# Optimization experiments

Hardware: AMD Instinct MI355X
Metric: run time of the kernel (lower is better)

## Reference

```python
import jax, jax.numpy as jnp
import numpy as np

EPS = 1e-6

def elu1(x):
    return jax.nn.elu(x) + 1.0

def causal_linear_attention(q, k, v, chunk=128):
    # q,k,v: [b,h,s,d]; standard (elu+1) linear attention with causal cumulative
    # normalization, computed chunk-wise with a lax.scan carrying the kv state.
    b, h, s, d = q.shape
    sq, sk = elu1(q), elu1(k)
    nc = s // chunk
    rs = lambda x: x.reshape(b, h, nc, chunk, d).transpose(2, 0, 1, 3, 4)  # [nc,b,h,L,d]
    sqc, skc, vc = rs(sq), rs(sk), rs(v)
    mask = jnp.tril(jnp.ones((chunk, chunk), dtype=q.dtype))

    def step(carry, xs):
        S, z = carry  # S: [b,h,d,d] running sum of k^T v; z: [b,h,d] running sum of k
        qc, kc, vcc = xs
        scores = jnp.einsum('bhid,bhjd->bhij', qc, kc) * mask
        num = jnp.einsum('bhij,bhje->bhie', scores, vcc) + jnp.einsum('bhid,bhde->bhie', qc, S)
        den = scores.sum(-1) + jnp.einsum('bhid,bhd->bhi', qc, z)
        out = num / jnp.clip(den, EPS)[..., None]
        S = S + jnp.einsum('bhjd,bhje->bhde', kc, vcc)
        z = z + kc.sum(2)
        return (S, z), out

    S0 = jnp.zeros((b, h, d, d), q.dtype)
    z0 = jnp.zeros((b, h, d), q.dtype)
    _, outs = jax.lax.scan(step, (S0, z0), (sqc, skc, vc))
    return outs.transpose(1, 2, 0, 3, 4).reshape(b, h, s, d)

def setup_inputs() -> dict:
    B, S, H, NH, NM = 2, 4096, 2048, 16, 4
    HD = H // NH
    key = jax.random.key(0)
    ks = jax.random.split(key, 12)
    p = lambda k, shp: (jax.random.normal(k, shp, dtype=jnp.float32) * 0.02)
    return {
        'hidden_states': jax.random.normal(ks[0], (B, S, H), dtype=jnp.float32),
        'w_q': p(ks[1], (H, H)),
        'w_k': p(ks[2], (H, H)),
        'w_v': p(ks[3], (H, H)),
        'w_o': p(ks[4], (H, H)),
        'eg_w1': p(ks[5], (H // 4, H)),
        'eg_b1': jnp.zeros((H // 4,), jnp.float32),
        'eg_w2': p(ks[6], (1, H // 4)),
        'eg_b2': jnp.zeros((1,), jnp.float32),
        'memory_gate': jnp.zeros((NH,), jnp.float32),
        'fine_memories': jax.random.uniform(ks[7], (NM, NH, HD, HD), dtype=jnp.float32) * 0.1,
        'fine_memory_norms': jax.random.uniform(ks[8], (NM, NH, HD), dtype=jnp.float32) + 0.1,
    }

def reference(hidden_states, w_q, w_k, w_v, w_o, eg_w1, eg_b1, eg_w2, eg_b2,
              memory_gate, fine_memories, fine_memory_norms):
    B, S, H = hidden_states.shape
    NH = memory_gate.shape[0]
    HD = H // NH
    split = lambda x: x.reshape(B, S, NH, HD).transpose(0, 2, 1, 3)  # [b,h,s,d]
    q = split(hidden_states @ w_q.T)
    k = split(hidden_states @ w_k.T)
    v = split(hidden_states @ w_v.T)
    sq = elu1(q)

    # coarse memory = sum of fine banks
    M = fine_memories.sum(0)            # [h,d,d]
    z = fine_memory_norms.sum(0)        # [h,d]
    a_c = jnp.einsum('bhsd,hde->bhse', sq, M)
    n_c = jnp.clip(jnp.einsum('bhsd,hd->bhs', sq, z), EPS)[..., None]
    out_coarse = jnp.where(z.sum() < EPS, 0.0, a_c / n_c)

    # fine-grained retrieval over banks, softmax-weighted by relevance
    a_f = jnp.einsum('bhsd,mhde->mbhse', sq, fine_memories)
    n_f = jnp.einsum('bhsd,mhd->mbhs', sq, fine_memory_norms)
    bank_dead = (fine_memory_norms.sum((1, 2)) < EPS)[:, None, None, None, None]
    outs = jnp.where(bank_dead, 0.0, a_f / jnp.clip(n_f, EPS)[..., None])
    rel = n_f.mean(-1)  # [m,b,h]
    w = jax.nn.softmax(rel, axis=0)[..., None, None]  # [m,b,h,1,1]
    out_fine = (outs * w).sum(0)

    # learned expansion gate from coarse representation
    coarse_repr = out_coarse.transpose(0, 2, 1, 3).reshape(B, S, H)
    gprob = jax.nn.sigmoid(jax.nn.relu(coarse_repr @ eg_w1.T + eg_b1) @ eg_w2.T + eg_b2)  # [b,s,1]
    exp_prob = gprob.transpose(0, 2, 1)[..., None]  # [b,1,s,1]

    memory_output = exp_prob * out_fine + (1.0 - exp_prob) * out_coarse
    local_output = causal_linear_attention(q, k, v)
    gate = jax.nn.sigmoid(memory_gate).reshape(1, NH, 1, 1)
    output = gate * memory_output + (1.0 - gate) * local_output
    output = output.transpose(0, 2, 1, 3).reshape(B, S, H)
    return output @ w_o.T
```

## Files before the change

### kernel.cpp

```cpp
#include <hip/hip_runtime.h>

typedef unsigned short ush;
typedef short s16x8 __attribute__((ext_vector_type(8)));
typedef float f32x4 __attribute__((ext_vector_type(4)));

#define Bv 2
#define Sv 4096
#define Hv 2048
#define NHv 16
#define HDv 128
#define NMv 4
#define Tv (Bv*Sv)
#define CHv 128
#define NCv (Sv/CHv)
#define EPSf 1e-6f
#define NTHc ((size_t)Tv*Hv)

__device__ __forceinline__ float b2f(ush u){ return __uint_as_float(((unsigned)u)<<16); }
__device__ __forceinline__ ush f2b(float f){
  unsigned x = __float_as_uint(f);
  return (ush)((x + 0x7fffu + ((x>>16)&1u)) >> 16);
}
__device__ __forceinline__ float lo16(unsigned u){ return b2f((ush)(u & 0xffffu)); }
__device__ __forceinline__ float hi16(unsigned u){ return b2f((ush)(u >> 16)); }
__device__ __forceinline__ unsigned pack2(float a, float b){ return (unsigned)f2b(a) | ((unsigned)f2b(b) << 16); }
__device__ __forceinline__ float elu1f(float x){ return x > 0.f ? x + 1.f : __expf(x); }
__device__ __forceinline__ float sigm(float x){ return 1.f/(1.f + __expf(-x)); }

__device__ __forceinline__ void gload_lds16(const ush* g, ush* l) {
  __builtin_amdgcn_global_load_lds((const __attribute__((address_space(1))) unsigned int*)g,
                                   (__attribute__((address_space(3))) unsigned int*)l, 16, 0, 0);
}

__global__ void probe_kernel(float* out, float val){ out[0] = val; }

__global__ __launch_bounds__(256)
void cvt_kernel(const float* __restrict__ in, ush* __restrict__ out, int n8)
{
  int i = blockIdx.x * 256 + threadIdx.x;
  if (i >= n8) return;
  const float4* p = (const float4*)in + (size_t)i*2;
  float4 x = p[0], y = p[1];
  ushort4 a; a.x=f2b(x.x); a.y=f2b(x.y); a.z=f2b(x.z); a.w=f2b(x.w);
  ushort4 b; b.x=f2b(y.x); b.y=f2b(y.y); b.z=f2b(y.z); b.w=f2b(y.w);
  *(ushort4*)(out + (size_t)i*8)     = a;
  *(ushort4*)(out + (size_t)i*8 + 4) = b;
}

__global__ __launch_bounds__(256)
void fmt_kernel(const float* __restrict__ fm, ush* __restrict__ fmt)
{
  int mh = blockIdx.x;
  const float* src = fm + (size_t)mh*HDv*HDv;
  ush* dst = fmt + (size_t)mh*HDv*HDv;
  __shared__ ush T[HDv][HDv+4];
  #pragma unroll 4
  for (int l = 0; l < 64; ++l) {
    int idx = threadIdx.x + l*256;
    int d = idx >> 7, e = idx & 127;
    T[d][e] = f2b(src[idx]);
  }
  __syncthreads();
  #pragma unroll 4
  for (int l = 0; l < 64; ++l) {
    int idx = threadIdx.x + l*256;
    int e = idx >> 7, d = idx & 127;
    dst[idx] = T[d][e];
  }
}

__global__ __launch_bounds__(256)
void tp_kernel(const ush* __restrict__ src, ush* __restrict__ dst)
{
  int blk = blockIdx.x;
  int st = blk & 31, bh = blk >> 5;
  int h = bh & 15, b = bh >> 4;
  size_t t0 = (size_t)b*Sv + st*128;
  int hcol = h*HDv;
  __shared__ __align__(16) ush T[128*128];
  int tid = threadIdx.x;
  #pragma unroll
  for (int l = 0; l < 8; ++l) {
    int idx = tid + l*256;
    int row = idx >> 4, c8 = (idx & 15) << 3;
    *(uint4*)(T + row*128 + c8) = *(const uint4*)(src + (t0 + row)*Hv + hcol + c8);
  }
  __syncthreads();
  #pragma unroll
  for (int l = 0; l < 8; ++l) {
    int idx = tid + l*256;
    int d = idx & 127, t8 = (idx >> 7) << 3;
    ush tmp[8];
    #pragma unroll
    for (int q = 0; q < 8; ++q) tmp[q] = T[(t8 + q)*128 + d];
    *(uint4*)(dst + ((size_t)bh*HDv + d)*Sv + st*128 + t8) = *(uint4*)tmp;
  }
}

template<int OBF, int EPQ>
__global__ __launch_bounds__(512)
void gemm9(const ush* __restrict__ A, const ush* __restrict__ B,
           ush* __restrict__ C0, ush* __restrict__ C1, ush* __restrict__ C2,
           float* __restrict__ Cf, int N, int K)
{
  __shared__ __align__(16) ush LDSm[65536];
  const int tid = threadIdx.x, lane = tid & 63, w = tid >> 6;
  const int wr = w >> 2, wn = w & 3;
  const int la = lane & 15, lk = lane >> 4;

  int bid = blockIdx.x;
  int NBX = N >> 8;
  int by, bx;
  if ((NBX & 7) == 0) {
    int bpx = NBX >> 3;
    int xcd = bid & 7;
    int idx = bid >> 3;
    bx = xcd*bpx + idx % bpx;
    by = idx / bpx;
  } else {
    bx = bid % NBX;
    by = bid / NBX;
  }
  int bm = by << 8, bn = bx << 8;

  auto stageA = [&](int t, int c){
    ush* Ad = LDSm + (t & 1)*32768 + c*8192;
    int kt = t << 6;
    #pragma unroll
    for (int l = 0; l < 2; ++l) {
      int u = tid + l*512;
      int row = u >> 3, sl = u & 7;
      gload_lds16(A + (size_t)(bm + c*128 + row)*K + kt + ((sl ^ (row & 7))*8),
                  Ad + (l*512 + w*64)*8);
    }
  };
  auto stageB = [&](int t, int c){
    ush* Bd = LDSm + (t & 1)*32768 + 16384 + c*8192;
    int kt = t << 6;
    #pragma unroll
    for (int l = 0; l < 2; ++l) {
      int u = tid + l*512;
      int row = u >> 3, sl = u & 7;
      gload_lds16(B + (size_t)(bn + c*128 + row)*K + kt + ((sl ^ (row & 7))*8),
                  Bd + (l*512 + w*64)*8);
    }
  };

  f32x4 acc[8][4];
  #pragma unroll
  for (int i = 0; i < 8; ++i)
    #pragma unroll
    for (int j = 0; j < 4; ++j) acc[i][j] = (f32x4){0.f,0.f,0.f,0.f};

  stageA(0,0); stageA(0,1); stageB(0,0); stageB(0,1);
  asm volatile("s_waitcnt vmcnt(0)" ::: "memory");
  __builtin_amdgcn_s_barrier();
  __builtin_amdgcn_sched_barrier(0);

  const int nt = K >> 6;
  for (int t = 0; t < nt; ++t) {
    const ush* Ab = LDSm + (t & 1)*32768;
    const ush* Bb = Ab + 16384;
    if (t + 1 < nt) { stageA(t+1, 0); stageA(t+1, 1); }
    s16x8 b0[4], a0[4];
    __builtin_amdgcn_s_setprio(1);
    #pragma unroll
    for (int g = 0; g < 4; ++g) {
      int br = wn*64 + g*16 + la;
      b0[g] = *(const s16x8*)(Bb + br*64 + ((lk ^ (br & 7))*8));
    }
    #pragma unroll
    for (int f = 0; f < 4; ++f) {
      int ar = wr*128 + f*16 + la;
      a0[f] = *(const s16x8*)(Ab + ar*64 + ((lk ^ (ar & 7))*8));
    }
    #pragma unroll
    for (int f = 0; f < 4; ++f)
      #pragma unroll
      for (int g = 0; g < 4; ++g)
        acc[f][g] = __builtin_amdgcn_mfma_f32_16x16x32_bf16(a0[f], b0[g], acc[f][g], 0, 0, 0);
    __builtin_amdgcn_s_setprio(0);
    if (t + 1 < nt) { stageB(t+1, 0); stageB(t+1, 1); }
    __builtin_amdgcn_s_setprio(1);
    #pragma unroll
    for (int f = 0; f < 4; ++f) {
      int ar = wr*128 + (f+4)*16 + la;
      a0[f] = *(const s16x8*)(Ab + ar*64 + ((lk ^ (ar & 7))*8));
    }
    #pragma unroll
    for (int f = 0; f < 4; ++f)
      #pragma unroll
      for (int g = 0; g < 4; ++g)
        acc[f+4][g] = __builtin_amdgcn_mfma_f32_16x16x32_bf16(a0[f], b0[g], acc[f+4][g], 0, 0, 0);
    int ks1 = 4 + lk;
    #pragma unroll
    for (int g = 0; g < 4; ++g) {
      int br = wn*64 + g*16 + la;
      b0[g] = *(const s16x8*)(Bb + br*64 + ((ks1 ^ (br & 7))*8));
    }
    #pragma unroll
    for (int f = 0; f < 4; ++f) {
      int ar = wr*128 + f*16 + la;
      a0[f] = *(const s16x8*)(Ab + ar*64 + ((ks1 ^ (ar & 7))*8));
    }
    #pragma unroll
    for (int f = 0; f < 4; ++f)
      #pragma unroll
      for (int g = 0; g < 4; ++g)
        acc[f][g] = __builtin_amdgcn_mfma_f32_16x16x32_bf16(a0[f], b0[g], acc[f][g], 0, 0, 0);
    #pragma unroll
    for (int f = 0; f < 4; ++f) {
      int ar = wr*128 + (f+4)*16 + la;
      a0[f] = *(const s16x8*)(Ab + ar*64 + ((ks1 ^ (ar & 7))*8));
    }
    #pragma unroll
    for (int f = 0; f < 4; ++f)
      #pragma unroll
      for (int g = 0; g < 4; ++g)
        acc[f+4][g] = __builtin_amdgcn_mfma_f32_16x16x32_bf16(a0[f], b0[g], acc[f+4][g], 0, 0, 0);
    __builtin_amdgcn_s_setprio(0);
    __builtin_amdgcn_sched_barrier(0);
    asm volatile("s_waitcnt vmcnt(0)" ::: "memory");
    __builtin_amdgcn_s_barrier();
    __builtin_amdgcn_sched_barrier(0);
  }

  int seg = bn >> 11;
  if (OBF) {
    ush* Cb = LDSm;
    ush* outp = (seg == 0) ? C0 : (seg == 1) ? C1 : C2;
    int col0 = bn & 2047;
    #pragma unroll
    for (int h = 0; h < 2; ++h) {
      if (h) __syncthreads();
      if (wr == h) {
        #pragma unroll
        for (int f = 0; f < 8; ++f)
          #pragma unroll
          for (int g = 0; g < 4; ++g)
            #pragma unroll
            for (int r = 0; r < 4; ++r) {
              int row = f*16 + lk*4 + r;
              int col = wn*64 + g*16 + la;
              float v = acc[f][g][r];
              if (EPQ == 1 && seg < 2) v = elu1f(v);
              Cb[row*264 + col] = f2b(v);
            }
      }
      __syncthreads();
      #pragma unroll
      for (int l = 0; l < 8; ++l) {
        int chunk = tid + l*512;
        int row = chunk >> 5, cc = chunk & 31;
        *(uint4*)(outp + (size_t)(bm + h*128 + row)*2048 + col0 + cc*8) = *(const uint4*)(Cb + row*264 + cc*8);
      }
    }
  } else {
    float* Cb = (float*)LDSm;
    #pragma unroll
    for (int h2 = 0; h2 < 4; ++h2) {
      if (h2) __syncthreads();
      if (wr == (h2 >> 1)) {
        #pragma unroll
        for (int f = 0; f < 4; ++f) {
          int fa = (h2 & 1)*4 + f;
          #pragma unroll
          for (int g = 0; g < 4; ++g)
            #pragma unroll
            for (int r = 0; r < 4; ++r) {
              int row = f*16 + lk*4 + r;
              int col = wn*64 + g*16 + la;
              Cb[row*260 + col] = acc[fa][g][r];
            }
        }
      }
      __syncthreads();
      #pragma unroll
      for (int l = 0; l < 8; ++l) {
        int chunk = tid + l*512;
        int row = chunk >> 6, cc = chunk & 63;
        *(float4*)(Cf + (size_t)(bm + h2*64 + row)*N + bn + cc*4) = *(const float4*)(Cb + row*260 + cc*4);
      }
    }
  }
}

template<int OBF, int EPQ>
__global__ __launch_bounds__(512)
void gemm8(const ush* __restrict__ A, const ush* __restrict__ B,
           const float* __restrict__ bias,
           ush* __restrict__ C0, ush* __restrict__ C1, ush* __restrict__ C2,
           float* __restrict__ Cf, int N, int K)
{
  __shared__ __align__(16) ush LDS[3*16384 + 3*8192];
  ush* Atb = LDS;
  ush* Btb = LDS + 3*16384;
  const int tid = threadIdx.x, lane = tid & 63, w = tid >> 6;
  const int wr = w >> 1, wn = w & 1;
  const int la = lane & 15, lk = lane >> 4;

  int bid = blockIdx.x;
  int NBX = N >> 7;
  int by, bx;
  if ((NBX & 7) == 0) {
    int bpx = NBX >> 3;
    int xcd = bid & 7;
    int idx = bid >> 3;
    bx = xcd*bpx + idx % bpx;
    by = idx / bpx;
  } else {
    bx = bid % NBX;
    by = bid / NBX;
  }
  int bm = by << 8, bn = bx << 7;

  auto stage = [&](int t){
    int kt = t << 6;
    ush* Ad = Atb + (t % 3) * 16384;
    ush* Bd = Btb + (t % 3) * 8192;
    #pragma unroll
    for (int c = 0; c < 4; ++c) {
      int idx = tid + c*512;
      int row = idx >> 3, sl = idx & 7;
      gload_lds16(A + (size_t)(bm + row)*K + kt + ((sl ^ (row & 7))*8),
                  Ad + (w*64 + c*512)*8);
    }
    #pragma unroll
    for (int c = 0; c < 2; ++c) {
      int idx = tid + c*512;
      int row = idx >> 3, sl = idx & 7;
      gload_lds16(B + (size_t)(bn + row)*K + kt + ((sl ^ (row & 7))*8),
                  Bd + (w*64 + c*512)*8);
    }
  };

  f32x4 acc[4][4];
  #pragma unroll
  for (int i = 0; i < 4; ++i)
    #pragma unroll
    for (int j = 0; j < 4; ++j) acc[i][j] = (f32x4){0.f,0.f,0.f,0.f};

  stage(0);
  stage(1);
  const int nt = 32;
  for (int t = 0; t < nt; ++t) {
    if (t < nt-2) {
      stage(t + 2);
      asm volatile("s_waitcnt vmcnt(12)" ::: "memory");
    } else if (t == nt-2) {
      asm volatile("s_waitcnt vmcnt(6)" ::: "memory");
    } else {
      asm volatile("s_waitcnt vmcnt(0)" ::: "memory");
    }
    __builtin_amdgcn_s_barrier();
    __builtin_amdgcn_sched_barrier(0);

    const ush* Ab = Atb + (t % 3) * 16384;
    const ush* Bb = Btb + (t % 3) * 8192;
    __builtin_amdgcn_s_setprio(1);
    #pragma unroll
    for (int kk = 0; kk < 2; ++kk) {
      s16x8 a[4], b[4];
      int ks = kk*4 + lk;
      #pragma unroll
      for (int f = 0; f < 4; ++f) {
        int ar = wr*64 + f*16 + la;
        a[f] = *(const s16x8*)(Ab + ar*64 + ((ks ^ (ar & 7))*8));
        int br = wn*64 + f*16 + la;
        b[f] = *(const s16x8*)(Bb + br*64 + ((ks ^ (br & 7))*8));
      }
      #pragma unroll
      for (int i = 0; i < 4; ++i)
        #pragma unroll
        for (int j = 0; j < 4; ++j)
          acc[i][j] = __builtin_amdgcn_mfma_f32_16x16x32_bf16(a[i], b[j], acc[i][j], 0, 0, 0);
    }
    __builtin_amdgcn_s_setprio(0);
    __builtin_amdgcn_sched_barrier(0);
    __builtin_amdgcn_s_barrier();
  }

  int seg = bn >> 11;
  if (OBF) {
    ush* Cb = LDS;
    #pragma unroll
    for (int i = 0; i < 4; ++i)
      #pragma unroll
      for (int j = 0; j < 4; ++j)
        #pragma unroll
        for (int r = 0; r < 4; ++r) {
          int row = wr*64 + i*16 + lk*4 + r;
          int col = wn*64 + j*16 + la;
          float v = acc[i][j][r];
          if (EPQ == 1 && seg < 2) v = elu1f(v);
          Cb[row*136 + col] = f2b(v);
        }
    __syncthreads();
    ush* outp = (seg == 0) ? C0 : (seg == 1) ? C1 : C2;
    int col0 = bn & 2047;
    #pragma unroll
    for (int l = 0; l < 8; ++l) {
      int chunk = tid + l*512;
      int row = chunk >> 4, cc = chunk & 15;
      *(uint4*)(outp + (size_t)(bm + row)*2048 + col0 + cc*8) = *(const uint4*)(Cb + row*136 + cc*8);
    }
  } else {
    float* Cb = (float*)LDS;
    #pragma unroll
    for (int i = 0; i < 4; ++i)
      #pragma unroll
      for (int j = 0; j < 4; ++j)
        #pragma unroll
        for (int r = 0; r < 4; ++r) {
          int row = wr*64 + i*16 + lk*4 + r;
          int col = wn*64 + j*16 + la;
          float v = acc[i][j][r];
          if (EPQ == 2) v = fmaxf(v + bias[bn + col], 0.f);
          Cb[row*132 + col] = v;
        }
    __syncthreads();
    #pragma unroll
    for (int l = 0; l < 16; ++l) {
      int chunk = tid + l*512;
      int row = chunk >> 5, cc = chunk & 31;
      *(float4*)(Cf + (size_t)(bm + row)*N + bn + cc*4) = *(const float4*)(Cb + row*132 + cc*4);
    }
  }
}

__global__ void prep_kernel(const float* __restrict__ norms, const float* __restrict__ mg,
                            float* __restrict__ zsum, float* __restrict__ gate)
{
  int idx = blockIdx.x * 256 + threadIdx.x;
  if (idx < NHv*HDv) {
    float s = 0.f;
    #pragma unroll
    for (int m = 0; m < NMv; ++m) s += norms[m*NHv*HDv + idx];
    zsum[idx] = s;
  }
  if (idx < NHv) gate[idx] = sigm(mg[idx]);
}

__global__ void prep2_kernel(const float* __restrict__ norms, float* __restrict__ bdead,
                             float* __restrict__ ztot, float* __restrict__ rel)
{
  int tid = threadIdx.x;
  float pm[NMv] = {0.f,0.f,0.f,0.f};
  for (int i = tid; i < NHv*HDv; i += 256)
    #pragma unroll
    for (int m = 0; m < NMv; ++m) pm[m] += norms[m*NHv*HDv + i];
  __shared__ float red[4][NMv];
  #pragma unroll
  for (int m = 0; m < NMv; ++m) {
    float v = pm[m];
    for (int off = 32; off; off >>= 1) v += __shfl_down(v, off, 64);
    if ((tid & 63) == 0) red[tid >> 6][m] = v;
  }
  __syncthreads();
  if (tid == 0) {
    float tot = 0.f;
    #pragma unroll
    for (int m = 0; m < NMv; ++m) {
      float s = red[0][m] + red[1][m] + red[2][m] + red[3][m];
      bdead[m] = (s < EPSf) ? 1.f : 0.f;
      tot += s;
    }
    ztot[0] = tot;
  }
  if (tid < NMv*Bv*NHv) rel[tid] = 0.f;
}

__global__ __launch_bounds__(256)
void nf_kernel(const ush* __restrict__ sq, const float* __restrict__ norms,
               const float* __restrict__ zsum, float* __restrict__ nf5,
               float* __restrict__ rel)
{
  int blk = blockIdx.x;
  int st = blk % (Sv/256);
  int bh = blk / (Sv/256);
  int h = bh & 15, b = bh >> 4;
  int tid = threadIdx.x;
  __shared__ float nrm[5][HDv];
  for (int i = tid; i < 5*HDv; i += 256) {
    int m = i / HDv, d = i % HDv;
    nrm[m][d] = (m < NMv) ? norms[(m*NHv + h)*HDv + d] : zsum[h*HDv + d];
  }
  __syncthreads();
  int s = st*256 + tid;
  size_t t = (size_t)b*Sv + s;
  const ush* qp = sq + t*Hv + h*HDv;
  float acc[5] = {0.f,0.f,0.f,0.f,0.f};
  #pragma unroll 4
  for (int d0 = 0; d0 < HDv; d0 += 8) {
    uint4 u = *(const uint4*)(qp + d0);
    float q[8];
    q[0]=lo16(u.x); q[1]=hi16(u.x); q[2]=lo16(u.y); q[3]=hi16(u.y);
    q[4]=lo16(u.z); q[5]=hi16(u.z); q[6]=lo16(u.w); q[7]=hi16(u.w);
    #pragma unroll
    for (int e = 0; e < 8; ++e)
      #pragma unroll
      for (int m = 0; m < 5; ++m) acc[m] = fmaf(q[e], nrm[m][d0+e], acc[m]);
  }
  #pragma unroll
  for (int m = 0; m < 5; ++m) nf5[((size_t)m*Bv*NHv + bh)*Sv + s] = acc[m];
  __shared__ float redl[4][NMv];
  #pragma unroll
  for (int m = 0; m < NMv; ++m) {
    float v = acc[m];
    for (int off = 32; off; off >>= 1) v += __shfl_down(v, off, 64);
    if ((tid & 63) == 0) redl[tid >> 6][m] = v;
  }
  __syncthreads();
  if (tid < NMv) {
    float sm = redl[0][tid] + redl[1][tid] + redl[2][tid] + redl[3][tid];
    atomicAdd(&rel[tid*Bv*NHv + bh], sm);
  }
}

__global__ void softmax_rel(const float* __restrict__ rel, float* __restrict__ wsm)
{
  int i = threadIdx.x;
  if (i >= Bv*NHv) return;
  float r[NMv], mx = -1e30f;
  #pragma unroll
  for (int m = 0; m < NMv; ++m) { r[m] = rel[m*Bv*NHv + i] / (float)Sv; mx = fmaxf(mx, r[m]); }
  float se = 0.f;
  #pragma unroll
  for (int m = 0; m < NMv; ++m) { r[m] = __expf(r[m] - mx); se += r[m]; }
  #pragma unroll
  for (int m = 0; m < NMv; ++m) wsm[m*Bv*NHv + i] = r[m] / se;
}

__global__ __launch_bounds__(512)
void finecoarse_mfma(const ush* __restrict__ sq, const ush* __restrict__ fmt,
                     const float* __restrict__ nf5, const float* __restrict__ wsm,
                     const float* __restrict__ bdead, const float* __restrict__ ztot,
                     ush* __restrict__ fineO, ush* __restrict__ coarseO)
{
  __shared__ __align__(16) ush Qs[2*128*64];
  __shared__ __align__(16) ush Fs[2*128*64];
  __shared__ float scl[NMv][128];
  __shared__ float csc[128];

  int blk = blockIdx.x;
  int tt = blk & 31; int bh = blk >> 5;
  int h = bh & 15, b = bh >> 4;
  size_t t0 = (size_t)b*Sv + tt*128;
  int hcol = h*HDv;
  int tid = threadIdx.x;
  int lane = tid & 63, w = tid >> 6;
  int wr = w >> 2, wc = w & 3;
  int srow = lane >> 3, sslot = lane & 7;
  int la = lane & 15, lk = lane >> 4;

  #pragma unroll
  for (int kh = 0; kh < 2; ++kh)
    #pragma unroll
    for (int r = 0; r < 2; ++r) {
      int row = r*64 + w*8 + srow;
      int kg = sslot ^ (row & 7);
      gload_lds16(sq + (t0 + row)*Hv + hcol + kh*64 + kg*8,
                  Qs + kh*8192 + (r*64 + w*8)*64);
    }
  if (tid < 128) {
    int s = tt*128 + tid;
    float nc = nf5[((size_t)4*Bv*NHv + bh)*Sv + s];
    csc[tid] = (ztot[0] >= EPSf) ? 1.f/fmaxf(nc, EPSf) : 0.f;
    #pragma unroll
    for (int m = 0; m < NMv; ++m) {
      float nfm = nf5[((size_t)m*Bv*NHv + bh)*Sv + s];
      scl[m][tid] = (bdead[m] > 0.5f) ? 0.f : wsm[m*Bv*NHv + bh]/fmaxf(nfm, EPSf);
    }
  }

  f32x4 accF[4][2], accC[4][2];
  #pragma unroll
  for (int i = 0; i < 4; ++i)
    #pragma unroll
    for (int j = 0; j < 2; ++j) { accF[i][j] = (f32x4){0,0,0,0}; accC[i][j] = (f32x4){0,0,0,0}; }

  for (int m = 0; m < NMv; ++m) {
    const ush* F = fmt + (size_t)(m*NHv + h)*HDv*HDv;
    #pragma unroll
    for (int kh = 0; kh < 2; ++kh)
      #pragma unroll
      for (int r = 0; r < 2; ++r) {
        int row = r*64 + w*8 + srow;
        int kg = sslot ^ (row & 7);
        gload_lds16(F + (size_t)row*HDv + kh*64 + kg*8,
                    Fs + kh*8192 + (r*64 + w*8)*64);
      }
    __syncthreads();
    f32x4 P[4][2];
    #pragma unroll
    for (int i = 0; i < 4; ++i)
      #pragma unroll
      for (int j = 0; j < 2; ++j) P[i][j] = (f32x4){0,0,0,0};
    #pragma unroll
    for (int kh = 0; kh < 2; ++kh)
      #pragma unroll
      for (int ks = 0; ks < 2; ++ks) {
        s16x8 a[4], bq[2];
        int kslot = ks*4 + lk;
        #pragma unroll
        for (int f = 0; f < 4; ++f) {
          int arow = wr*64 + f*16 + la;
          a[f] = *(const s16x8*)(Qs + kh*8192 + arow*64 + ((kslot ^ (arow & 7))*8));
        }
        #pragma unroll
        for (int f = 0; f < 2; ++f) {
          int brow = wc*32 + f*16 + la;
          bq[f] = *(const s16x8*)(Fs + kh*8192 + brow*64 + ((kslot ^ (brow & 7))*8));
        }
        #pragma unroll
        for (int i = 0; i < 4; ++i)
          #pragma unroll
          for (int j = 0; j < 2; ++j)
            P[i][j] = __builtin_amdgcn_mfma_f32_16x16x32_bf16(a[i], bq[j], P[i][j], 0, 0, 0);
      }
    #pragma unroll
    for (int i = 0; i < 4; ++i) {
      float sm[4];
      #pragma unroll
      for (int r = 0; r < 4; ++r) sm[r] = scl[m][wr*64 + i*16 + lk*4 + r];
      #pragma unroll
      for (int j = 0; j < 2; ++j)
        #pragma unroll
        for (int r = 0; r < 4; ++r) {
          accF[i][j][r] = fmaf(sm[r], P[i][j][r], accF[i][j][r]);
          accC[i][j][r] += P[i][j][r];
        }
    }
    __syncthreads();
  }
  #pragma unroll
  for (int i = 0; i < 4; ++i)
    #pragma unroll
    for (int r = 0; r < 4; ++r) {
      int row = wr*64 + i*16 + lk*4 + r;
      float cs = csc[row];
      size_t gro = (t0 + row)*Hv + hcol;
      #pragma unroll
      for (int j = 0; j < 2; ++j) {
        int col = wc*32 + j*16 + la;
        fineO[gro + col]   = f2b(accF[i][j][r]);
        coarseO[gro + col] = f2b(accC[i][j][r]*cs);
      }
    }
}

__global__ __launch_bounds__(64)
void gprob_kernel(const float* __restrict__ g1, const float* __restrict__ w2,
                  const float* __restrict__ b2, float* __restrict__ gprob)
{
  int t = blockIdx.x, l = threadIdx.x;
  float s = 0.f;
  #pragma unroll
  for (int i = l; i < Hv/4; i += 64) s = fmaf(g1[(size_t)t*(Hv/4) + i], w2[i], s);
  for (int off = 32; off; off >>= 1) s += __shfl_down(s, off, 64);
  if (l == 0) gprob[t] = sigm(s + b2[0]);
}

__global__ __launch_bounds__(512)
void kv_chunk_mfma(const ush* __restrict__ kT, const ush* __restrict__ vT,
                   float* __restrict__ KVc, float* __restrict__ zc)
{
  __shared__ __align__(16) ush Vt[128*128];
  __shared__ __align__(16) ush Kt[128*128];
  int blk = blockIdx.x;
  int c = blk & 31, bh = blk >> 5;
  const ush* kg = kT + (size_t)bh*HDv*Sv + c*CHv;
  const ush* vg = vT + (size_t)bh*HDv*Sv + c*CHv;
  int tid = threadIdx.x, lane = tid & 63, w = tid >> 6;
  int wr = w >> 2, wc = w & 3;
  int la = lane & 15, lk = lane >> 4;
  int srow4 = lane >> 4, sslot = lane & 15;

  #pragma unroll
  for (int r = 0; r < 4; ++r) {
    int row = r*32 + w*4 + srow4;
    int slot = sslot ^ (row & 7);
    gload_lds16(vg + (size_t)row*Sv + slot*8, Vt + (r*32 + w*4)*128);
    gload_lds16(kg + (size_t)row*Sv + slot*8, Kt + (r*32 + w*4)*128);
  }
  __syncthreads();

  if (tid < 128) {
    float zacc = 0.f;
    int rx = tid & 7;
    #pragma unroll
    for (int s = 0; s < 16; ++s) {
      const ush* p = Kt + tid*128 + ((s ^ rx)*8);
      #pragma unroll
      for (int q = 0; q < 8; ++q) zacc += b2f(p[q]);
    }
    zc[(size_t)blk*HDv + tid] = zacc;
  }

  f32x4 acc[4][2];
  #pragma unroll
  for (int i = 0; i < 4; ++i)
    #pragma unroll
    for (int j = 0; j < 2; ++j) acc[i][j] = (f32x4){0,0,0,0};
  #pragma unroll
  for (int kw = 0; kw < 4; ++kw) {
    s16x8 a[4], b[2];
    int slot = kw*4 + lk;
    #pragma unroll
    for (int f = 0; f < 4; ++f) {
      int ar = wr*64 + f*16 + la;
      a[f] = *(const s16x8*)(Vt + ar*128 + ((slot ^ (ar & 7))*8));
    }
    #pragma unroll
    for (int f = 0; f < 2; ++f) {
      int br = wc*32 + f*16 + la;
      b[f] = *(const s16x8*)(Kt + br*128 + ((slot ^ (br & 7))*8));
    }
    #pragma unroll
    for (int i = 0; i < 4; ++i)
      #pragma unroll
      for (int j = 0; j < 2; ++j)
        acc[i][j] = __builtin_amdgcn_mfma_f32_16x16x32_bf16(a[i], b[j], acc[i][j], 0, 0, 0);
  }
  size_t obase = (size_t)blk*(HDv*HDv);
  #pragma unroll
  for (int i = 0; i < 4; ++i)
    #pragma unroll
    for (int j = 0; j < 2; ++j)
      #pragma unroll
      for (int r = 0; r < 4; ++r) {
        int e = wr*64 + i*16 + lk*4 + r;
        int d = wc*32 + j*16 + la;
        KVc[obase + e*HDv + d] = acc[i][j][r];
      }
}

__global__ __launch_bounds__(256)
void scan_kernel(const float* __restrict__ KVc, ush* __restrict__ kvt, float* __restrict__ zc)
{
  int blk = blockIdx.x;
  int dg = blk & 7; int bh = blk >> 3;
  int tid = threadIdx.x;
  float Sreg[8];
  #pragma unroll
  for (int k = 0; k < 8; ++k) Sreg[k] = 0.f;
  float zreg = 0.f;
  for (int c = 0; c < NCv; ++c) {
    size_t base = ((size_t)bh*NCv + c)*(HDv*HDv) + dg*2048;
    #pragma unroll
    for (int k = 0; k < 8; ++k) {
      size_t idx = base + tid + k*256;
      float tmp = KVc[idx];
      kvt[idx] = f2b(Sreg[k]);
      Sreg[k] += tmp;
    }
    if (dg == 0 && tid < HDv) {
      size_t zb = ((size_t)bh*NCv + c)*HDv + tid;
      float tmp = zc[zb];
      zc[zb] = zreg;
      zreg += tmp;
    }
  }
}

__global__ __launch_bounds__(512)
void attn_chunk_mfma(const ush* __restrict__ sq, const ush* __restrict__ sk,
                     const ush* __restrict__ vT, const ush* __restrict__ kvt,
                     const float* __restrict__ zc, ush* __restrict__ outl)
{
  __shared__ __align__(16) ush Qs[128*128];
  __shared__ __align__(16) ush Ks[128*128];
  __shared__ __align__(16) ush Vs[128*128];
  __shared__ __align__(16) ush Ss[128*128];
  __shared__ float densP[4][128];
  __shared__ float dens[128];

  int blk = blockIdx.x;
  int c = blk & 31, bh = blk >> 5;
  int h = bh & 15, b = bh >> 4;
  size_t t0 = (size_t)b*Sv + c*CHv;
  int hcol = h*HDv;
  int tid = threadIdx.x, lane = tid & 63, w = tid >> 6;
  int wr = w >> 2, wc = w & 3;
  int la = lane & 15, lk = lane >> 4;
  int srow4 = lane >> 4, sslot = lane & 15;
  const float* zcg = zc + (size_t)blk*HDv;

  const ush* qg = sq + t0*Hv + hcol;
  const ush* kg = sk + t0*Hv + hcol;
  const ush* vg = vT + (size_t)bh*HDv*Sv + c*CHv;
  const ush* sg = kvt + (size_t)blk*(HDv*HDv);
  #pragma unroll
  for (int r = 0; r < 4; ++r) {
    int row = r*32 + w*4 + srow4;
    int slot = sslot ^ (row & 7);
    int lb = (r*32 + w*4)*128;
    gload_lds16(qg + (size_t)row*Hv + slot*8, Qs + lb);
    gload_lds16(kg + (size_t)row*Hv + slot*8, Ks + lb);
    gload_lds16(vg + (size_t)row*Sv + slot*8, Vs + lb);
    gload_lds16(sg + row*HDv + slot*8, Ss + lb);
  }
  __syncthreads();

  f32x4 sc[4][2];
  #pragma unroll
  for (int i = 0; i < 4; ++i)
    #pragma unroll
    for (int j = 0; j < 2; ++j) sc[i][j] = (f32x4){0,0,0,0};
  #pragma unroll
  for (int kw = 0; kw < 4; ++kw) {
    s16x8 a[4], b[2];
    int slot = kw*4 + lk;
    #pragma unroll
    for (int f = 0; f < 4; ++f) {
      int ar = wr*64 + f*16 + la;
      a[f] = *(const s16x8*)(Qs + ar*128 + ((slot ^ (ar & 7))*8));
    }
    #pragma unroll
    for (int f = 0; f < 2; ++f) {
      int br = wc*32 + f*16 + la;
      b[f] = *(const s16x8*)(Ks + br*128 + ((slot ^ (br & 7))*8));
    }
    #pragma unroll
    for (int i = 0; i < 4; ++i)
      #pragma unroll
      for (int j = 0; j < 2; ++j)
        sc[i][j] = __builtin_amdgcn_mfma_f32_16x16x32_bf16(a[i], b[j], sc[i][j], 0, 0, 0);
  }
  __syncthreads();
  #pragma unroll
  for (int i = 0; i < 4; ++i)
    #pragma unroll
    for (int j = 0; j < 2; ++j)
      #pragma unroll
      for (int r = 0; r < 4; ++r) {
        int ii = wr*64 + i*16 + lk*4 + r;
        int jj = wc*32 + j*16 + la;
        float v = (jj <= ii) ? sc[i][j][r] : 0.f;
        Ks[ii*128 + (((jj >> 3) ^ (ii & 7))*8) + (jj & 7)] = f2b(v);
      }
  __syncthreads();

  {
    int row = tid & 127, qt = tid >> 7;
    int rx = row & 7;
    float s = 0.f;
    #pragma unroll
    for (int s8 = 0; s8 < 4; ++s8) {
      int slot = qt*4 + s8;
      const ush* p  = Ks + row*128 + ((slot ^ rx)*8);
      const ush* pq = Qs + row*128 + ((slot ^ rx)*8);
      #pragma unroll
      for (int q = 0; q < 8; ++q) s += b2f(p[q]);
      #pragma unroll
      for (int q = 0; q < 8; ++q) s = fmaf(b2f(pq[q]), zcg[slot*8 + q], s);
    }
    densP[qt][row] = s;
  }
  __syncthreads();
  if (tid < 128)
    dens[tid] = fmaxf(densP[0][tid] + densP[1][tid] + densP[2][tid] + densP[3][tid], EPSf);
  __syncthreads();

  f32x4 acc[4][2];
  #pragma unroll
  for (int i = 0; i < 4; ++i)
    #pragma unroll
    for (int j = 0; j < 2; ++j) acc[i][j] = (f32x4){0,0,0,0};
  #pragma unroll
  for (int kw = 0; kw < 4; ++kw) {
    s16x8 a[4], b[2];
    int slot = kw*4 + lk;
    #pragma unroll
    for (int f = 0; f < 4; ++f) {
      int ar = wr*64 + f*16 + la;
      a[f] = *(const s16x8*)(Ks + ar*128 + ((slot ^ (ar & 7))*8));
    }
    #pragma unroll
    for (int f = 0; f < 2; ++f) {
      int br = wc*32 + f*16 + la;
      b[f] = *(const s16x8*)(Vs + br*128 + ((slot ^ (br & 7))*8));
    }
    #pragma unroll
    for (int i = 0; i < 4; ++i)
      #pragma unroll
      for (int j = 0; j < 2; ++j)
        acc[i][j] = __builtin_amdgcn_mfma_f32_16x16x32_bf16(a[i], b[j], acc[i][j], 0, 0, 0);
  }
  #pragma unroll
  for (int kw = 0; kw < 4; ++kw) {
    s16x8 a[4], b[2];
    int slot = kw*4 + lk;
    #pragma unroll
    for (int f = 0; f < 4; ++f) {
      int ar = wr*64 + f*16 + la;
      a[f] = *(const s16x8*)(Qs + ar*128 + ((slot ^ (ar & 7))*8));
    }
    #pragma unroll
    for (int f = 0; f < 2; ++f) {
      int br = wc*32 + f*16 + la;
      b[f] = *(const s16x8*)(Ss + br*128 + ((slot ^ (br & 7))*8));
    }
    #pragma unroll
    for (int i = 0; i < 4; ++i)
      #pragma unroll
      for (int j = 0; j < 2; ++j)
        acc[i][j] = __builtin_amdgcn_mfma_f32_16x16x32_bf16(a[i], b[j], acc[i][j], 0, 0, 0);
  }
  #pragma unroll
  for (int i = 0; i < 4; ++i)
    #pragma unroll
    for (int r = 0; r < 4; ++r) {
      int ii = wr*64 + i*16 + lk*4 + r;
      float inv = 1.f / dens[ii];
      ush* orow = outl + (t0 + ii)*Hv + hcol;
      #pragma unroll
      for (int j = 0; j < 2; ++j) {
        int ee = wc*32 + j*16 + la;
        orow[ee] = f2b(acc[i][j][r]*inv);
      }
    }
}

__global__ __launch_bounds__(256)
void combine_kernel(const ush* __restrict__ fine, const ush* __restrict__ coarse,
                    const ush* __restrict__ local, const float* __restrict__ gprob,
                    const float* __restrict__ gate, ush* __restrict__ comb)
{
  size_t idx = (size_t)blockIdx.x * 256 + threadIdx.x;
  if (idx >= NTHc/8) return;
  size_t fi = idx * 8;
  int t = (int)(fi / Hv);
  int h = (int)((fi % Hv) >> 7);
  float g = gate[h];
  float p = gprob[t];
  uint4 uf = *(const uint4*)(fine + fi);
  uint4 uc = *(const uint4*)(coarse + fi);
  uint4 ul = *(const uint4*)(local + fi);
  uint4 o;
  unsigned* ufp = (unsigned*)&uf; unsigned* ucp = (unsigned*)&uc;
  unsigned* ulp = (unsigned*)&ul; unsigned* op = (unsigned*)&o;
  #pragma unroll
  for (int wq = 0; wq < 4; ++wq) {
    float f0 = lo16(ufp[wq]), f1 = hi16(ufp[wq]);
    float c0 = lo16(ucp[wq]), c1 = hi16(ucp[wq]);
    float l0 = lo16(ulp[wq]), l1 = hi16(ulp[wq]);
    float o0 = g*(p*f0 + (1.f-p)*c0) + (1.f-g)*l0;
    float o1 = g*(p*f1 + (1.f-p)*c1) + (1.f-g)*l1;
    op[wq] = pack2(o0, o1);
  }
  *(uint4*)(comb + fi) = o;
}

extern "C" void kernel_launch(void* const* d_in, const int* in_sizes, int n_in,
                              void* d_out, int out_size, void* d_ws, size_t ws_size,
                              hipStream_t stream)
{
  (void)in_sizes; (void)n_in; (void)out_size;
  const float* hs    = (const float*)d_in[0];
  const float* w_q   = (const float*)d_in[1];
  const float* w_k   = (const float*)d_in[2];
  const float* w_v   = (const float*)d_in[3];
  const float* w_o   = (const float*)d_in[4];
  const float* eg_w1 = (const float*)d_in[5];
  const float* eg_b1 = (const float*)d_in[6];
  const float* eg_w2 = (const float*)d_in[7];
  const float* eg_b2 = (const float*)d_in[8];
  const float* mg    = (const float*)d_in[9];
  const float* fm    = (const float*)d_in[10];
  const float* norms = (const float*)d_in[11];

  probe_kernel<<<1, 1, 0, stream>>>((float*)d_out, (float)(ws_size >> 20));

  char* W = (char*)d_ws;
  size_t o = 0;
  auto take = [&](size_t bytes) -> char* {
    char* p = W + o;
    o += (bytes + 255) & ~(size_t)255;
    return p;
  };
  ush* hs_bf = (ush*)take(NTHc * 2);
  ush* kT = hs_bf;
  ush* local_bf = hs_bf;
  char* R2 = take(NTHc * 4);
  ush* wq_bf = (ush*)R2;
  ush* wk_bf = (ush*)(R2 + (size_t)Hv*Hv*2);
  ush* wv_bf = (ush*)(R2 + (size_t)Hv*Hv*4);
  float* kvc = (float*)R2;
  ush* fine_bf = (ush*)R2;
  float* g1 = (float*)(R2 + NTHc*2);
  ush* wo_bf   = (ush*)take((size_t)Hv*Hv*2);
  ush* egw1_bf = (ush*)take((size_t)(Hv/4)*Hv*2);
  ush* sq_bf = (ush*)take(NTHc * 2);  ush* comb = sq_bf;
  ush* sk_bf = (ush*)take(NTHc * 2);
  ush* v_bf  = (ush*)take(NTHc * 2);
  ush* kvt_bf = v_bf;
  ush* vT = (ush*)take(NTHc * 2);
  ush* coarse_bf = vT;
  float* zcb  = (float*)take((size_t)Bv*NHv*NCv*HDv * 4);
  float* nf5  = (float*)take((size_t)5*Bv*NHv*Sv * 4);
  ush* fmt_bf = (ush*)take((size_t)NMv*NHv*HDv*HDv * 2);
  float* rel  = (float*)take(NMv*Bv*NHv * 4);
  float* wsm  = (float*)take(NMv*Bv*NHv * 4);
  float* gprob= (float*)take((size_t)Tv * 4);
  float* zsum = (float*)take(NHv*HDv * 4);
  float* gate = (float*)take(NHv * 4);
  float* bdead= (float*)take(NMv * 4);
  float* ztot = (float*)take(4);
  if (ws_size < o) return;

  cvt_kernel<<<(int)(NTHc/8/256), 256, 0, stream>>>(hs, hs_bf, (int)(NTHc/8));
  cvt_kernel<<<(int)((size_t)Hv*Hv/8/256), 256, 0, stream>>>(w_q, wq_bf, Hv*Hv/8);
  cvt_kernel<<<(int)((size_t)Hv*Hv/8/256), 256, 0, stream>>>(w_k, wk_bf, Hv*Hv/8);
  cvt_kernel<<<(int)((size_t)Hv*Hv/8/256), 256, 0, stream>>>(w_v, wv_bf, Hv*Hv/8);
  cvt_kernel<<<(int)((size_t)Hv*Hv/8/256), 256, 0, stream>>>(w_o, wo_bf, Hv*Hv/8);
  cvt_kernel<<<(int)((size_t)(Hv/4)*Hv/8/256), 256, 0, stream>>>(eg_w1, egw1_bf, (Hv/4)*Hv/8);
  fmt_kernel<<<NMv*NHv, 256, 0, stream>>>(fm, fmt_bf);

  prep_kernel<<<(NHv*HDv + 255)/256, 256, 0, stream>>>(norms, mg, zsum, gate);
  prep2_kernel<<<1, 256, 0, stream>>>(norms, bdead, ztot, rel);

  gemm9<1,1><<<(6144/256)*(Tv/256), 512, 0, stream>>>(hs_bf, wq_bf,
                                                      sq_bf, sk_bf, v_bf, nullptr, 6144, Hv);

  tp_kernel<<<Bv*NHv*32, 256, 0, stream>>>(sk_bf, kT);
  tp_kernel<<<Bv*NHv*32, 256, 0, stream>>>(v_bf, vT);

  nf_kernel<<<Bv*NHv*(Sv/256), 256, 0, stream>>>(sq_bf, norms, zsum, nf5, rel);
  softmax_rel<<<1, 64, 0, stream>>>(rel, wsm);

  kv_chunk_mfma<<<Bv*NHv*NCv, 512, 0, stream>>>(kT, vT, kvc, zcb);
  scan_kernel<<<Bv*NHv*8, 256, 0, stream>>>(kvc, kvt_bf, zcb);
  attn_chunk_mfma<<<Bv*NHv*NCv, 512, 0, stream>>>(sq_bf, sk_bf, vT, kvt_bf, zcb, local_bf);

  finecoarse_mfma<<<Bv*NHv*32, 512, 0, stream>>>(sq_bf, fmt_bf, nf5, wsm, bdead, ztot, fine_bf, coarse_bf);

  gemm8<0,2><<<(512/128)*(Tv/256), 512, 0, stream>>>(coarse_bf, egw1_bf, eg_b1,
                                                     nullptr, nullptr, nullptr, g1, 512, Hv);
  gprob_kernel<<<Tv, 64, 0, stream>>>(g1, eg_w2, eg_b2, gprob);

  combine_kernel<<<(int)(NTHc/8/256), 256, 0, stream>>>(fine_bf, coarse_bf, local_bf, gprob, gate, comb);

  gemm9<0,0><<<(2048/256)*(Tv/256), 512, 0, stream>>>(comb, wo_bf,
                                                      nullptr, nullptr, nullptr, (float*)d_out, 2048, Hv);
}
```

Baseline: 557.7 us.

## Restructure GEMM LDS layout into K-halves with finer-grained staged prefetch

The bf16 GEMM's shared-memory tiles now hold two 32-wide K halves, each 256 rows by 32 columns with a 4-way XOR swizzle, instead of two 128-row halves spanning the full 64-wide K. Global-to-LDS prefetch for the next tile is split into four quarter-stages interleaved between the four MFMA phases. Partial vmcnt waits and barriers before each phase replace the single full drain at the end of each iteration. The aim is to overlap memory traffic with compute more evenly, at the cost of more barriers per iteration and a smaller swizzle that may raise LDS bank conflicts.

```diff
diff --git a/kernel.cpp b/kernel.cpp
--- a/kernel.cpp
+++ b/kernel.cpp
@@ -99,9 +99,9 @@
 
 template<int OBF, int EPQ>
 __global__ __launch_bounds__(512)
-void gemm9(const ush* __restrict__ A, const ush* __restrict__ B,
-           ush* __restrict__ C0, ush* __restrict__ C1, ush* __restrict__ C2,
-           float* __restrict__ Cf, int N, int K)
+void gemm10(const ush* __restrict__ A, const ush* __restrict__ B,
+            ush* __restrict__ C0, ush* __restrict__ C1, ush* __restrict__ C2,
+            float* __restrict__ Cf, int N, int K)
 {
   __shared__ __align__(16) ush LDSm[65536];
   const int tid = threadIdx.x, lane = tid & 63, w = tid >> 6;
@@ -123,26 +123,26 @@
   }
   int bm = by << 8, bn = bx << 8;
 
-  auto stageA = [&](int t, int c){
-    ush* Ad = LDSm + (t & 1)*32768 + c*8192;
+  auto stageA = [&](int t, int kh){
+    ush* Ad = LDSm + (t & 1)*32768 + kh*8192;
     int kt = t << 6;
     #pragma unroll
     for (int l = 0; l < 2; ++l) {
       int u = tid + l*512;
-      int row = u >> 3, sl = u & 7;
-      gload_lds16(A + (size_t)(bm + c*128 + row)*K + kt + ((sl ^ (row & 7))*8),
-                  Ad + (l*512 + w*64)*8);
+      int row = u >> 2, s2 = u & 3;
+      int kg = (kh << 2) + (s2 ^ ((row >> 1) & 3));
+      gload_lds16(A + (size_t)(bm + row)*K + kt + kg*8, Ad + (l*512 + w*64)*8);
     }
   };
-  auto stageB = [&](int t, int c){
-    ush* Bd = LDSm + (t & 1)*32768 + 16384 + c*8192;
+  auto stageB = [&](int t, int kh){
+    ush* Bd = LDSm + (t & 1)*32768 + 16384 + kh*8192;
     int kt = t << 6;
     #pragma unroll
     for (int l = 0; l < 2; ++l) {
       int u = tid + l*512;
-      int row = u >> 3, sl = u & 7;
-      gload_lds16(B + (size_t)(bn + c*128 + row)*K + kt + ((sl ^ (row & 7))*8),
-                  Bd + (l*512 + w*64)*8);
+      int row = u >> 2, s2 = u & 3;
+      int kg = (kh << 2) + (s2 ^ ((row >> 1) & 3));
+      gload_lds16(B + (size_t)(bn + row)*K + kt + kg*8, Bd + (l*512 + w*64)*8);
     }
   };
 
@@ -152,78 +152,101 @@
     #pragma unroll
     for (int j = 0; j < 4; ++j) acc[i][j] = (f32x4){0.f,0.f,0.f,0.f};
 
-  stageA(0,0); stageA(0,1); stageB(0,0); stageB(0,1);
-  asm volatile("s_waitcnt vmcnt(0)" ::: "memory");
-  __builtin_amdgcn_s_barrier();
-  __builtin_amdgcn_sched_barrier(0);
+  stageA(0,0); stageB(0,0); stageA(0,1); stageB(0,1);
 
   const int nt = K >> 6;
   for (int t = 0; t < nt; ++t) {
-    const ush* Ab = LDSm + (t & 1)*32768;
-    const ush* Bb = Ab + 16384;
-    if (t + 1 < nt) { stageA(t+1, 0); stageA(t+1, 1); }
-    s16x8 b0[4], a0[4];
-    __builtin_amdgcn_s_setprio(1);
+    const int bb = (t & 1)*32768;
+    const bool st = (t + 1 < nt);
+    s16x8 a0[4], a1[4], b0[4];
+
+    asm volatile("s_waitcnt vmcnt(4)" ::: "memory");
+    __builtin_amdgcn_s_barrier();
+    __builtin_amdgcn_sched_barrier(0);
     #pragma unroll
     for (int g = 0; g < 4; ++g) {
       int br = wn*64 + g*16 + la;
-      b0[g] = *(const s16x8*)(Bb + br*64 + ((lk ^ (br & 7))*8));
+      b0[g] = *(const s16x8*)(LDSm + bb + 16384 + br*32 + ((lk ^ ((br>>1)&3))*8));
     }
     #pragma unroll
     for (int f = 0; f < 4; ++f) {
       int ar = wr*128 + f*16 + la;
-      a0[f] = *(const s16x8*)(Ab + ar*64 + ((lk ^ (ar & 7))*8));
-    }
+      a0[f] = *(const s16x8*)(LDSm + bb + ar*32 + ((lk ^ ((ar>>1)&3))*8));
+    }
+    if (st) stageA(t+1, 0);
+    asm volatile("s_waitcnt lgkmcnt(0)" ::: "memory");
+    __builtin_amdgcn_sched_barrier(0);
+    __builtin_amdgcn_s_setprio(1);
     #pragma unroll
     for (int f = 0; f < 4; ++f)
       #pragma unroll
       for (int g = 0; g < 4; ++g)
         acc[f][g] = __builtin_amdgcn_mfma_f32_16x16x32_bf16(a0[f], b0[g], acc[f][g], 0, 0, 0);
     __builtin_amdgcn_s_setprio(0);
-    if (t + 1 < nt) { stageB(t+1, 0); stageB(t+1, 1); }
-    __builtin_amdgcn_s_setprio(1);
+
+    __builtin_amdgcn_s_barrier();
+    __builtin_amdgcn_sched_barrier(0);
     #pragma unroll
     for (int f = 0; f < 4; ++f) {
       int ar = wr*128 + (f+4)*16 + la;
-      a0[f] = *(const s16x8*)(Ab + ar*64 + ((lk ^ (ar & 7))*8));
-    }
+      a1[f] = *(const s16x8*)(LDSm + bb + ar*32 + ((lk ^ ((ar>>1)&3))*8));
+    }
+    if (st) stageB(t+1, 0);
+    asm volatile("s_waitcnt lgkmcnt(0)" ::: "memory");
+    __builtin_amdgcn_sched_barrier(0);
+    __builtin_amdgcn_s_setprio(1);
     #pragma unroll
     for (int f = 0; f < 4; ++f)
       #pragma unroll
       for (int g = 0; g < 4; ++g)
-        acc[f+4][g] = __builtin_amdgcn_mfma_f32_16x16x32_bf16(a0[f], b0[g], acc[f+4][g], 0, 0, 0);
-    int ks1 = 4 + lk;
+        acc[f+4][g] = __builtin_amdgcn_mfma_f32_16x16x32_bf16(a1[f], b0[g], acc[f+4][g], 0, 0, 0);
+    __builtin_amdgcn_s_setprio(0);
+
+    if (st) { asm volatile("s_waitcnt vmcnt(4)" ::: "memory"); }
+    else    { asm volatile("s_waitcnt vmcnt(0)" ::: "memory"); }
+    __builtin_amdgcn_s_barrier();
+    __builtin_amdgcn_sched_barrier(0);
     #pragma unroll
     for (int g = 0; g < 4; ++g) {
       int br = wn*64 + g*16 + la;
-      b0[g] = *(const s16x8*)(Bb + br*64 + ((ks1 ^ (br & 7))*8));
+      b0[g] = *(const s16x8*)(LDSm + bb + 16384 + 8192 + br*32 + ((lk ^ ((br>>1)&3))*8));
     }
     #pragma unroll
     for (int f = 0; f < 4; ++f) {
       int ar = wr*128 + f*16 + la;
-      a0[f] = *(const s16x8*)(Ab + ar*64 + ((ks1 ^ (ar & 7))*8));
-    }
+      a0[f] = *(const s16x8*)(LDSm + bb + 8192 + ar*32 + ((lk ^ ((ar>>1)&3))*8));
+    }
+    if (st) stageA(t+1, 1);
+    asm volatile("s_waitcnt lgkmcnt(0)" ::: "memory");
+    __builtin_amdgcn_sched_barrier(0);
+    __builtin_amdgcn_s_setprio(1);
     #pragma unroll
     for (int f = 0; f < 4; ++f)
       #pragma unroll
       for (int g = 0; g < 4; ++g)
         acc[f][g] = __builtin_amdgcn_mfma_f32_16x16x32_bf16(a0[f], b0[g], acc[f][g], 0, 0, 0);
+    __builtin_amdgcn_s_setprio(0);
+
+    __builtin_amdgcn_s_barrier();
+    __builtin_amdgcn_sched_barrier(0);
     #pragma unroll
     for (int f = 0; f < 4; ++f) {
       int ar = wr*128 + (f+4)*16 + la;
-      a0[f] = *(const s16x8*)(Ab + ar*64 + ((ks1 ^ (ar & 7))*8));
-    }
+      a1[f] = *(const s16x8*)(LDSm + bb + 8192 + ar*32 + ((lk ^ ((ar>>1)&3))*8));
+    }
+    if (st) stageB(t+1, 1);
+    asm volatile("s_waitcnt lgkmcnt(0)" ::: "memory");
+    __builtin_amdgcn_sched_barrier(0);
+    __builtin_amdgcn_s_setprio(1);
     #pragma unroll
     for (int f = 0; f < 4; ++f)
       #pragma unroll
       for (int g = 0; g < 4; ++g)
-        acc[f+4][g] = __builtin_amdgcn_mfma_f32_16x16x32_bf16(a0[f], b0[g], acc[f+4][g], 0, 0, 0);
+        acc[f+4][g] = __builtin_amdgcn_mfma_f32_16x16x32_bf16(a1[f], b0[g], acc[f+4][g], 0, 0, 0);
     __builtin_amdgcn_s_setprio(0);
-    __builtin_amdgcn_sched_barrier(0);
-    asm volatile("s_waitcnt vmcnt(0)" ::: "memory");
-    __builtin_amdgcn_s_barrier();
-    __builtin_amdgcn_sched_barrier(0);
-  }
+  }
+  asm volatile("s_waitcnt vmcnt(0)" ::: "memory");
+  __syncthreads();
 
   int seg = bn >> 11;
   if (OBF) {
@@ -1020,8 +1043,8 @@
   prep_kernel<<<(NHv*HDv + 255)/256, 256, 0, stream>>>(norms, mg, zsum, gate);
   prep2_kernel<<<1, 256, 0, stream>>>(norms, bdead, ztot, rel);
 
-  gemm9<1,1><<<(6144/256)*(Tv/256), 512, 0, stream>>>(hs_bf, wq_bf,
-                                                      sq_bf, sk_bf, v_bf, nullptr, 6144, Hv);
+  gemm10<1,1><<<(6144/256)*(Tv/256), 512, 0, stream>>>(hs_bf, wq_bf,
+                                                       sq_bf, sk_bf, v_bf, nullptr, 6144, Hv);
 
   tp_kernel<<<Bv*NHv*32, 256, 0, stream>>>(sk_bf, kT);
   tp_kernel<<<Bv*NHv*32, 256, 0, stream>>>(v_bf, vT);
@@ -1041,6 +1064,6 @@
 
   combine_kernel<<<(int)(NTHc/8/256), 256, 0, stream>>>(fine_bf, coarse_bf, local_bf, gprob, gate, comb);
 
-  gemm9<0,0><<<(2048/256)*(Tv/256), 512, 0, stream>>>(comb, wo_bf,
-                                                      nullptr, nullptr, nullptr, (float*)d_out, 2048, Hv);
-}
+  gemm10<0,0><<<(2048/256)*(Tv/256), 512, 0, stream>>>(comb, wo_bf,
+                                                       nullptr, nullptr, nullptr, (float*)d_out, 2048, Hv);
+}
```

Result: slower. 575.1 us (+3.1%).
